# Kernel optimization log

Measured on AMD Instinct MI355X. Metric: run time of the kernel, lower is better.

The kernel has to match this reference:

```python
import jax, jax.numpy as jnp
import numpy as np

N, D, C = 100000, 384, 8


def setup_inputs() -> dict:
    key = jax.random.key(0)
    k1, k2, k3, k4 = jax.random.split(key, 4)
    Y = jax.random.normal(k1, (N, D), dtype=jnp.float32)
    O = jax.random.bernoulli(k2, 0.9, (N, D))  # observation mask
    # learned VB parameters (as held in the nn.Parameters of VBPCA)
    mbar = 0.1 * jax.random.normal(k3, (D,), dtype=jnp.float32)
    wbar = 0.1 * jax.random.normal(k4, (D, C), dtype=jnp.float32)
    Sigmaw = jnp.broadcast_to(jnp.eye(C, dtype=jnp.float32), (D, C, C))
    vy = jnp.float32(1.0)
    return {"Y": Y, "O": O, "mbar": mbar, "wbar": wbar, "Sigmaw": Sigmaw, "vy": vy}


def reference(Y, O, mbar, wbar, Sigmaw, vy):
    O_ = O.astype(Y.dtype)            # [N, D]
    Y = jnp.nan_to_num(Y)
    # per-channel rank-c outer product plus Sigmaw: baddbmm(Sigmaw, wbar[:,:,None], wbar[:,None,:])
    OwwSw = Sigmaw + wbar[:, :, None] * wbar[:, None, :]            # [D, C, C]
    # accumulate over observed channels: [N, D] @ [D, C*C] -> [N, C, C]
    A = (O_ @ OwwSw.reshape(D, C * C)).reshape(-1, C, C)
    Ic = jnp.eye(C, dtype=Y.dtype)
    Sigma_xn = vy * jnp.linalg.inv(vy * Ic[None] + A)               # [N, C, C]
    # xbarn = einsum('nlk,ni,ik,ni->nl', Sigma_xn/vy, O_, wbar, Y - mbar)
    t = O_ * (Y - mbar)                                             # [N, D]
    proj = t @ wbar                                                 # [N, C]
    xbarn = jnp.einsum('nlk,nk->nl', Sigma_xn / vy, proj)           # [N, C]
    return xbarn, Sigma_xn
```

## Files before the change

### kernel.cpp

```cpp
#include <hip/hip_runtime.h>

#define NN 100000
#define DD 384
#define CC 8
#define ROWS 64

typedef unsigned int uint;
typedef _Float16 half8 __attribute__((ext_vector_type(8)));
typedef float floatx4 __attribute__((ext_vector_type(4)));

__device__ __forceinline__ constexpr int TIDX(int i, int j) { return i * (i + 1) / 2 + j; }

__device__ __forceinline__ uint pkh2(float a, float b) {
  return __builtin_bit_cast(uint, __builtin_amdgcn_cvt_pkrtz(a, b));
}

__global__ __launch_bounds__(64) void vbpca_prep(
    const float* __restrict__ wbar, const float* __restrict__ Sigmaw,
    uint4* __restrict__ bfrag) {
  const int l = threadIdx.x;
  const int kt = blockIdx.x;
  const int kgrp = l >> 4;
#pragma unroll
  for (int ct = 0; ct < 3; ++ct) {
    const int col = ct * 16 + (l & 15);
    int ii = 0;
#pragma unroll
    for (int t = 0; t < 7; ++t) {
      if ((ii + 1) * (ii + 2) / 2 <= col && ii < 7) ++ii;
    }
    const int jj = col - ii * (ii + 1) / 2;
    float v[8];
#pragma unroll
    for (int j = 0; j < 8; ++j) {
      const int d = kt * 32 + kgrp * 8 + j;
      float val;
      if (col < 36) {
        val = Sigmaw[(size_t)d * 64 + ii * 8 + jj] + wbar[d * 8 + ii] * wbar[d * 8 + jj];
      } else if (col < 44) {
        val = wbar[d * 8 + (col - 36)];
      } else {
        val = 0.f;
      }
      v[j] = val;
    }
    uint4 u;
    u.x = pkh2(v[0], v[1]); u.y = pkh2(v[2], v[3]);
    u.z = pkh2(v[4], v[5]); u.w = pkh2(v[6], v[7]);
    bfrag[(kt * 3 + ct) * 64 + l] = u;
  }
}

__global__ __launch_bounds__(256, 4) void vbpca_main(
    const float* __restrict__ Y, const int* __restrict__ O,
    const uint4* __restrict__ bfrag, const float* __restrict__ mbar,
    const float* __restrict__ vyp, float* __restrict__ out) {
  __shared__ float smemf[6656];
  float* mbar_l = smemf;
  float* scat_l = smemf + 384;
  float* sigst = smemf + 384;
  float* xbst = smemf + 384 + 4160;

  const int tid = threadIdx.x;
  const int wu = __builtin_amdgcn_readfirstlane((int)(tid >> 6));
  const int l = tid & 63;

  for (int i = tid; i < DD; i += 256) mbar_l[i] = mbar[i];
  __syncthreads();

  const int rt0 = blockIdx.x * ROWS + wu * 16;
  int gr0 = rt0 + ((l & 15) >> 1);
  gr0 = gr0 < NN ? gr0 : NN - 1;
  int gr1 = rt0 + 8 + ((l & 15) >> 1);
  gr1 = gr1 < NN ? gr1 : NN - 1;
  const float tsel = (float)(l & 1);
  const float osel = 1.f - tsel;
  const int kgo = (l >> 4) * 8;

  const float* __restrict__ Yr0 = Y + (size_t)gr0 * DD;
  const int* __restrict__ Or0 = O + (size_t)gr0 * DD;
  const float* __restrict__ Yr1 = Y + (size_t)gr1 * DD;
  const int* __restrict__ Or1 = O + (size_t)gr1 * DD;

  floatx4 accA[3], accB[3];
#pragma unroll
  for (int j = 0; j < 3; ++j) {
    accA[j] = (floatx4){0.f, 0.f, 0.f, 0.f};
    accB[j] = (floatx4){0.f, 0.f, 0.f, 0.f};
  }

#define GATHER_FRAG(YR, OR, KT, FRAG)                                       \
  {                                                                         \
    const int kb = (KT) * 32 + kgo;                                         \
    const float4 ylo = *reinterpret_cast<const float4*>((YR) + kb);         \
    const float4 yhi = *reinterpret_cast<const float4*>((YR) + kb + 4);     \
    const int4 olo = *reinterpret_cast<const int4*>((OR) + kb);             \
    const int4 ohi = *reinterpret_cast<const int4*>((OR) + kb + 4);         \
    const float4 mlo = *reinterpret_cast<const float4*>(mbar_l + kb);       \
    const float4 mhi = *reinterpret_cast<const float4*>(mbar_l + kb + 4);   \
    const float v0 = (float)olo.x * fmaf(tsel, ylo.x - mlo.x, osel);        \
    const float v1 = (float)olo.y * fmaf(tsel, ylo.y - mlo.y, osel);        \
    const float v2 = (float)olo.z * fmaf(tsel, ylo.z - mlo.z, osel);        \
    const float v3 = (float)olo.w * fmaf(tsel, ylo.w - mlo.w, osel);        \
    const float v4 = (float)ohi.x * fmaf(tsel, yhi.x - mhi.x, osel);        \
    const float v5 = (float)ohi.y * fmaf(tsel, yhi.y - mhi.y, osel);        \
    const float v6 = (float)ohi.z * fmaf(tsel, yhi.z - mhi.z, osel);        \
    const float v7 = (float)ohi.w * fmaf(tsel, yhi.w - mhi.w, osel);        \
    uint4 fu;                                                               \
    fu.x = pkh2(v0, v1); fu.y = pkh2(v2, v3);                               \
    fu.z = pkh2(v4, v5); fu.w = pkh2(v6, v7);                               \
    FRAG = __builtin_bit_cast(half8, fu);                                   \
  }

#define MTILE_LOOP(YR, OR, ACC)                                             \
  {                                                                         \
    uint4 bf0 = bfrag[0 * 64 + l];                                          \
    uint4 bf1 = bfrag[1 * 64 + l];                                          \
    uint4 bf2 = bfrag[2 * 64 + l];                                          \
    _Pragma("unroll") for (int kt = 0; kt < 12; ++kt) {                     \
      half8 av;                                                             \
      GATHER_FRAG(YR, OR, kt, av);                                          \
      uint4 nb0, nb1, nb2;                                                  \
      if (kt < 11) {                                                        \
        nb0 = bfrag[((kt + 1) * 3 + 0) * 64 + l];                           \
        nb1 = bfrag[((kt + 1) * 3 + 1) * 64 + l];                           \
        nb2 = bfrag[((kt + 1) * 3 + 2) * 64 + l];                           \
      }                                                                     \
      ACC[0] = __builtin_amdgcn_mfma_f32_16x16x32_f16(                      \
          av, __builtin_bit_cast(half8, bf0), ACC[0], 0, 0, 0);             \
      ACC[1] = __builtin_amdgcn_mfma_f32_16x16x32_f16(                      \
          av, __builtin_bit_cast(half8, bf1), ACC[1], 0, 0, 0);             \
      ACC[2] = __builtin_amdgcn_mfma_f32_16x16x32_f16(                      \
          av, __builtin_bit_cast(half8, bf2), ACC[2], 0, 0, 0);             \
      bf0 = nb0; bf1 = nb1; bf2 = nb2;                                      \
    }                                                                       \
  }

  MTILE_LOOP(Yr0, Or0, accA);
  MTILE_LOOP(Yr1, Or1, accB);

  __syncthreads();

#pragma unroll
  for (int ct = 0; ct < 3; ++ct) {
#pragma unroll
    for (int reg = 0; reg < 4; ++reg) {
      const int m = (l >> 4) * 4 + reg;
      scat_l[(wu * 32 + m) * 49 + ct * 16 + (l & 15)] = accA[ct][reg];
      scat_l[(wu * 32 + 16 + m) * 49 + ct * 16 + (l & 15)] = accB[ct][reg];
    }
  }
  __syncthreads();

  float a[36], pr[CC];
  if (tid < 64) {
#pragma unroll
    for (int k = 0; k < 36; ++k) a[k] = scat_l[(2 * tid) * 49 + k];
#pragma unroll
    for (int j = 0; j < CC; ++j) pr[j] = scat_l[(2 * tid + 1) * 49 + 36 + j];
  }
  __syncthreads();

  if (tid < 64) {
    const int row = tid;
    const float vy = *vyp;

    float L[36];
#pragma unroll
    for (int j = 0; j < CC; ++j) {
      float s = a[TIDX(j, j)] + vy;
#pragma unroll
      for (int k = 0; k < CC; ++k) {
        if (k < j) s -= L[TIDX(j, k)] * L[TIDX(j, k)];
      }
      const float dj = sqrtf(s);
      L[TIDX(j, j)] = dj;
      const float invdj = 1.0f / dj;
#pragma unroll
      for (int i = j + 1; i < CC; ++i) {
        float tt = a[TIDX(i, j)];
#pragma unroll
        for (int k = 0; k < CC; ++k) {
          if (k < j) tt -= L[TIDX(i, k)] * L[TIDX(j, k)];
        }
        L[TIDX(i, j)] = tt * invdj;
      }
    }

    float invd[CC];
#pragma unroll
    for (int i = 0; i < CC; ++i) invd[i] = 1.0f / L[TIDX(i, i)];
    float Li[36];
#pragma unroll
    for (int j = 0; j < CC; ++j) {
      Li[TIDX(j, j)] = invd[j];
#pragma unroll
      for (int i = j + 1; i < CC; ++i) {
        float s = 0.f;
#pragma unroll
        for (int k = 0; k < CC; ++k) {
          if (k >= j && k < i) s += L[TIDX(i, k)] * Li[TIDX(k, j)];
        }
        Li[TIDX(i, j)] = -s * invd[i];
      }
    }

    float sig[36];
#pragma unroll
    for (int i = 0; i < CC; ++i) {
#pragma unroll
      for (int j = 0; j <= i; ++j) {
        float s = 0.f;
#pragma unroll
        for (int k = 0; k < CC; ++k) {
          if (k >= i) s += Li[TIDX(k, i)] * Li[TIDX(k, j)];
        }
        sig[TIDX(i, j)] = vy * s;
      }
    }

    float uvec[CC];
#pragma unroll
    for (int i = 0; i < CC; ++i) {
      float s = 0.f;
#pragma unroll
      for (int j = 0; j < CC; ++j) {
        if (j <= i) s += Li[TIDX(i, j)] * pr[j];
      }
      uvec[i] = s;
    }
#pragma unroll
    for (int ll = 0; ll < CC; ++ll) {
      float s = 0.f;
#pragma unroll
      for (int i = 0; i < CC; ++i) {
        if (i >= ll) s += Li[TIDX(i, ll)] * uvec[i];
      }
      xbst[row * 9 + ll] = s;
    }
#pragma unroll
    for (int i = 0; i < CC; ++i) {
#pragma unroll
      for (int j = 0; j < CC; ++j) {
        sigst[row * 65 + i * 8 + j] = (j <= i) ? sig[TIDX(i, j)] : sig[TIDX(j, i)];
      }
    }
  }
  __syncthreads();

  const int valid = (NN - blockIdx.x * ROWS < ROWS) ? (NN - blockIdx.x * ROWS) : ROWS;
  float* __restrict__ sig_out = out + (size_t)NN * CC + (size_t)blockIdx.x * ROWS * 64;
  for (int f = tid; f < valid * 64; f += 256) {
    sig_out[f] = sigst[(f >> 6) * 65 + (f & 63)];
  }
  float* __restrict__ xb_out = out + (size_t)blockIdx.x * ROWS * CC;
  for (int f = tid; f < valid * 8; f += 256) {
    xb_out[f] = xbst[(f >> 3) * 9 + (f & 7)];
  }
}

extern "C" void kernel_launch(void* const* d_in, const int* in_sizes, int n_in,
                              void* d_out, int out_size, void* d_ws, size_t ws_size,
                              hipStream_t stream) {
  const float* Y = (const float*)d_in[0];
  const int* O = (const int*)d_in[1];
  const float* mbar = (const float*)d_in[2];
  const float* wbar = (const float*)d_in[3];
  const float* Sigmaw = (const float*)d_in[4];
  const float* vyp = (const float*)d_in[5];
  float* out = (float*)d_out;
  uint4* bfrag = (uint4*)d_ws;

  vbpca_prep<<<12, 64, 0, stream>>>(wbar, Sigmaw, bfrag);
  vbpca_main<<<(NN + ROWS - 1) / ROWS, 256, 0, stream>>>(Y, O, bfrag, mbar, vyp, out);
}
```

Baseline: 89.89 us.

## Stage Y and O tiles through LDS with async double-buffered global_load_lds

Each wave used to gather its Y and O fragments straight from global memory inside the MFMA loop. Now the wave's row tiles are prefetched into a per-wave, XOR-swizzled LDS double buffer using async global-to-LDS loads, and fragments are read from LDS. The aim is to overlap global memory latency with MFMA work and to get coalesced 16-byte row loads. In exchange, shared memory grows to about 50KB per block and launch bounds drop to 3 blocks per CU. Correctness depends on the compiler inserting the right vmcnt waits before LDS reads and before each buffer is overwritten.

```diff
diff --git a/kernel.cpp b/kernel.cpp
--- a/kernel.cpp
+++ b/kernel.cpp
@@ -51,15 +51,16 @@
   }
 }
 
-__global__ __launch_bounds__(256, 4) void vbpca_main(
+__global__ __launch_bounds__(256, 3) void vbpca_main(
     const float* __restrict__ Y, const int* __restrict__ O,
     const uint4* __restrict__ bfrag, const float* __restrict__ mbar,
     const float* __restrict__ vyp, float* __restrict__ out) {
-  __shared__ float smemf[6656];
-  float* mbar_l = smemf;
-  float* scat_l = smemf + 384;
-  float* sigst = smemf + 384;
-  float* xbst = smemf + 384 + 4160;
+  __shared__ uint smem[12672];
+  uint* tile = smem;
+  float* mbar_l = (float*)(smem + 12288);
+  float* scat_l = (float*)smem;
+  float* sigst = (float*)smem;
+  float* xbst = (float*)smem + 4160;
 
   const int tid = threadIdx.x;
   const int wu = __builtin_amdgcn_readfirstlane((int)(tid >> 6));
@@ -68,19 +69,31 @@
   for (int i = tid; i < DD; i += 256) mbar_l[i] = mbar[i];
   __syncthreads();
 
+  uint* wbuf = tile + wu * 3072;
   const int rt0 = blockIdx.x * ROWS + wu * 16;
-  int gr0 = rt0 + ((l & 15) >> 1);
-  gr0 = gr0 < NN ? gr0 : NN - 1;
-  int gr1 = rt0 + 8 + ((l & 15) >> 1);
-  gr1 = gr1 < NN ? gr1 : NN - 1;
   const float tsel = (float)(l & 1);
   const float osel = 1.f - tsel;
-  const int kgo = (l >> 4) * 8;
-
-  const float* __restrict__ Yr0 = Y + (size_t)gr0 * DD;
-  const int* __restrict__ Or0 = O + (size_t)gr0 * DD;
-  const float* __restrict__ Yr1 = Y + (size_t)gr1 * DD;
-  const int* __restrict__ Or1 = O + (size_t)gr1 * DD;
+
+#define GLOAD16(GSRC, LDST)                                                  \
+  __builtin_amdgcn_global_load_lds(                                          \
+      (const __attribute__((address_space(1))) void*)(GSRC),                 \
+      (__attribute__((address_space(3))) void*)(LDST), 16, 0, 0)
+
+#define ISSUE(M, S, BUF)                                                     \
+  {                                                                          \
+    _Pragma("unroll") for (int i = 0; i < 3; ++i) {                          \
+      const int p = i * 64 + l;                                              \
+      const int r = p / 24;                                                  \
+      const int c4 = (p - r * 24) ^ (r & 7);                                 \
+      int row = rt0 + (M)*8 + r;                                             \
+      row = row < NN ? row : NN - 1;                                         \
+      const size_t goff = (size_t)row * 96 + (S)*24 + c4;                    \
+      GLOAD16(reinterpret_cast<const float4*>(Y) + goff,                     \
+              wbuf + (BUF)*1536 + i * 256 + l * 4);                          \
+      GLOAD16(reinterpret_cast<const int4*>(O) + goff,                       \
+              wbuf + (BUF)*1536 + 768 + i * 256 + l * 4);                    \
+    }                                                                        \
+  }
 
   floatx4 accA[3], accB[3];
 #pragma unroll
@@ -88,56 +101,82 @@
     accA[j] = (floatx4){0.f, 0.f, 0.f, 0.f};
     accB[j] = (floatx4){0.f, 0.f, 0.f, 0.f};
   }
-
-#define GATHER_FRAG(YR, OR, KT, FRAG)                                       \
-  {                                                                         \
-    const int kb = (KT) * 32 + kgo;                                         \
-    const float4 ylo = *reinterpret_cast<const float4*>((YR) + kb);         \
-    const float4 yhi = *reinterpret_cast<const float4*>((YR) + kb + 4);     \
-    const int4 olo = *reinterpret_cast<const int4*>((OR) + kb);             \
-    const int4 ohi = *reinterpret_cast<const int4*>((OR) + kb + 4);         \
-    const float4 mlo = *reinterpret_cast<const float4*>(mbar_l + kb);       \
-    const float4 mhi = *reinterpret_cast<const float4*>(mbar_l + kb + 4);   \
-    const float v0 = (float)olo.x * fmaf(tsel, ylo.x - mlo.x, osel);        \
-    const float v1 = (float)olo.y * fmaf(tsel, ylo.y - mlo.y, osel);        \
-    const float v2 = (float)olo.z * fmaf(tsel, ylo.z - mlo.z, osel);        \
-    const float v3 = (float)olo.w * fmaf(tsel, ylo.w - mlo.w, osel);        \
-    const float v4 = (float)ohi.x * fmaf(tsel, yhi.x - mhi.x, osel);        \
-    const float v5 = (float)ohi.y * fmaf(tsel, yhi.y - mhi.y, osel);        \
-    const float v6 = (float)ohi.z * fmaf(tsel, yhi.z - mhi.z, osel);        \
-    const float v7 = (float)ohi.w * fmaf(tsel, yhi.w - mhi.w, osel);        \
-    uint4 fu;                                                               \
-    fu.x = pkh2(v0, v1); fu.y = pkh2(v2, v3);                               \
-    fu.z = pkh2(v4, v5); fu.w = pkh2(v6, v7);                               \
-    FRAG = __builtin_bit_cast(half8, fu);                                   \
-  }
-
-#define MTILE_LOOP(YR, OR, ACC)                                             \
-  {                                                                         \
-    uint4 bf0 = bfrag[0 * 64 + l];                                          \
-    uint4 bf1 = bfrag[1 * 64 + l];                                          \
-    uint4 bf2 = bfrag[2 * 64 + l];                                          \
-    _Pragma("unroll") for (int kt = 0; kt < 12; ++kt) {                     \
-      half8 av;                                                             \
-      GATHER_FRAG(YR, OR, kt, av);                                          \
-      uint4 nb0, nb1, nb2;                                                  \
-      if (kt < 11) {                                                        \
-        nb0 = bfrag[((kt + 1) * 3 + 0) * 64 + l];                           \
-        nb1 = bfrag[((kt + 1) * 3 + 1) * 64 + l];                           \
-        nb2 = bfrag[((kt + 1) * 3 + 2) * 64 + l];                           \
-      }                                                                     \
-      ACC[0] = __builtin_amdgcn_mfma_f32_16x16x32_f16(                      \
-          av, __builtin_bit_cast(half8, bf0), ACC[0], 0, 0, 0);             \
-      ACC[1] = __builtin_amdgcn_mfma_f32_16x16x32_f16(                      \
-          av, __builtin_bit_cast(half8, bf1), ACC[1], 0, 0, 0);             \
-      ACC[2] = __builtin_amdgcn_mfma_f32_16x16x32_f16(                      \
-          av, __builtin_bit_cast(half8, bf2), ACC[2], 0, 0, 0);             \
-      bf0 = nb0; bf1 = nb1; bf2 = nb2;                                      \
-    }                                                                       \
-  }
-
-  MTILE_LOOP(Yr0, Or0, accA);
-  MTILE_LOOP(Yr1, Or1, accB);
+  uint4 bf0, bf1, bf2;
+
+#define FRAG(S, J, BUF, AV)                                                  \
+  half8 AV;                                                                  \
+  {                                                                          \
+    const int ktg = (S)*3 + (J);                                             \
+    const int r = (l & 15) >> 1;                                             \
+    const int c4a = (J)*8 + (l >> 4) * 2;                                    \
+    const uint* bb = wbuf + (BUF)*1536;                                      \
+    const float4 ylo = *reinterpret_cast<const float4*>(                     \
+        bb + (r * 24 + ((c4a) ^ (r & 7))) * 4);                              \
+    const float4 yhi = *reinterpret_cast<const float4*>(                     \
+        bb + (r * 24 + ((c4a + 1) ^ (r & 7))) * 4);                          \
+    const int4 olo = *reinterpret_cast<const int4*>(                         \
+        bb + 768 + (r * 24 + ((c4a) ^ (r & 7))) * 4);                        \
+    const int4 ohi = *reinterpret_cast<const int4*>(                         \
+        bb + 768 + (r * 24 + ((c4a + 1) ^ (r & 7))) * 4);                    \
+    const float4 mlo =                                                       \
+        *reinterpret_cast<const float4*>(mbar_l + ktg * 32 + (l >> 4) * 8);  \
+    const float4 mhi = *reinterpret_cast<const float4*>(                     \
+        mbar_l + ktg * 32 + (l >> 4) * 8 + 4);                               \
+    const float v0 = (float)olo.x * fmaf(tsel, ylo.x - mlo.x, osel);         \
+    const float v1 = (float)olo.y * fmaf(tsel, ylo.y - mlo.y, osel);         \
+    const float v2 = (float)olo.z * fmaf(tsel, ylo.z - mlo.z, osel);         \
+    const float v3 = (float)olo.w * fmaf(tsel, ylo.w - mlo.w, osel);         \
+    const float v4 = (float)ohi.x * fmaf(tsel, yhi.x - mhi.x, osel);         \
+    const float v5 = (float)ohi.y * fmaf(tsel, yhi.y - mhi.y, osel);         \
+    const float v6 = (float)ohi.z * fmaf(tsel, yhi.z - mhi.z, osel);         \
+    const float v7 = (float)ohi.w * fmaf(tsel, yhi.w - mhi.w, osel);         \
+    uint4 fu;                                                                \
+    fu.x = pkh2(v0, v1); fu.y = pkh2(v2, v3);                                \
+    fu.z = pkh2(v4, v5); fu.w = pkh2(v6, v7);                                \
+    AV = __builtin_bit_cast(half8, fu);                                      \
+  }
+
+#define KT_BODY(S, J, BUF, ACC)                                              \
+  {                                                                          \
+    FRAG(S, J, BUF, av);                                                     \
+    const int ktn = (S)*3 + (J) + 1;                                         \
+    uint4 nb0, nb1, nb2;                                                     \
+    if (ktn < 12) {                                                          \
+      nb0 = bfrag[(ktn * 3 + 0) * 64 + l];                                   \
+      nb1 = bfrag[(ktn * 3 + 1) * 64 + l];                                   \
+      nb2 = bfrag[(ktn * 3 + 2) * 64 + l];                                   \
+    }                                                                        \
+    ACC[0] = __builtin_amdgcn_mfma_f32_16x16x32_f16(                         \
+        av, __builtin_bit_cast(half8, bf0), ACC[0], 0, 0, 0);                \
+    ACC[1] = __builtin_amdgcn_mfma_f32_16x16x32_f16(                         \
+        av, __builtin_bit_cast(half8, bf1), ACC[1], 0, 0, 0);                \
+    ACC[2] = __builtin_amdgcn_mfma_f32_16x16x32_f16(                         \
+        av, __builtin_bit_cast(half8, bf2), ACC[2], 0, 0, 0);                \
+    bf0 = nb0; bf1 = nb1; bf2 = nb2;                                         \
+  }
+
+#define BPRELOAD()                                                           \
+  bf0 = bfrag[0 * 64 + l];                                                   \
+  bf1 = bfrag[1 * 64 + l];                                                   \
+  bf2 = bfrag[2 * 64 + l];
+
+#define STEP(S, BUF, ACC)                                                    \
+  KT_BODY(S, 0, BUF, ACC);                                                   \
+  KT_BODY(S, 1, BUF, ACC);                                                   \
+  KT_BODY(S, 2, BUF, ACC);
+
+  ISSUE(0, 0, 0);
+  ISSUE(0, 1, 1);
+  BPRELOAD();
+  STEP(0, 0, accA);  ISSUE(0, 2, 0);
+  STEP(1, 1, accA);  ISSUE(0, 3, 1);
+  STEP(2, 0, accA);  ISSUE(1, 0, 0);
+  STEP(3, 1, accA);  ISSUE(1, 1, 1);
+  BPRELOAD();
+  STEP(0, 0, accB);  ISSUE(1, 2, 0);
+  STEP(1, 1, accB);  ISSUE(1, 3, 1);
+  STEP(2, 0, accB);
+  STEP(3, 1, accB);
 
   __syncthreads();
 
```

Result: slower. 94.13 us (+4.7%).

## Split MFMA accumulation and per-row Cholesky solve into separate kernels

Applied to the files above, without the earlier changes.

The fused kernel is split in two. The MFMA reduction kernel now handles 32 rows per block, writes the 44 packed moments per row to a workspace buffer, and declares higher occupancy through launch bounds. A second kernel reads the workspace and runs the 8x8 Cholesky inverse and the projection, 64 rows per block. This removes the serial single-wave solve tail from the bandwidth-bound MFMA kernel and allows more concurrent blocks. The cost is an extra kernel launch plus a round trip of about 19 MB through global memory.

```diff
diff --git a/kernel.cpp b/kernel.cpp
--- a/kernel.cpp
+++ b/kernel.cpp
@@ -3,7 +3,6 @@
 #define NN 100000
 #define DD 384
 #define CC 8
-#define ROWS 64
 
 typedef unsigned int uint;
 typedef _Float16 half8 __attribute__((ext_vector_type(8)));
@@ -51,16 +50,11 @@
   }
 }
 
-__global__ __launch_bounds__(256, 4) void vbpca_main(
+__global__ __launch_bounds__(256, 8) void vbpca_mfma(
     const float* __restrict__ Y, const int* __restrict__ O,
     const uint4* __restrict__ bfrag, const float* __restrict__ mbar,
-    const float* __restrict__ vyp, float* __restrict__ out) {
-  __shared__ float smemf[6656];
-  float* mbar_l = smemf;
-  float* scat_l = smemf + 384;
-  float* sigst = smemf + 384;
-  float* xbst = smemf + 384 + 4160;
-
+    float* __restrict__ cws) {
+  __shared__ float mbar_l[DD];
   const int tid = threadIdx.x;
   const int wu = __builtin_amdgcn_readfirstlane((int)(tid >> 6));
   const int l = tid & 63;
@@ -68,102 +62,100 @@
   for (int i = tid; i < DD; i += 256) mbar_l[i] = mbar[i];
   __syncthreads();
 
-  const int rt0 = blockIdx.x * ROWS + wu * 16;
-  int gr0 = rt0 + ((l & 15) >> 1);
-  gr0 = gr0 < NN ? gr0 : NN - 1;
-  int gr1 = rt0 + 8 + ((l & 15) >> 1);
-  gr1 = gr1 < NN ? gr1 : NN - 1;
+  const int R0 = blockIdx.x * 32 + wu * 8;
+  const int gr = R0 + ((l & 15) >> 1);
   const float tsel = (float)(l & 1);
   const float osel = 1.f - tsel;
   const int kgo = (l >> 4) * 8;
 
-  const float* __restrict__ Yr0 = Y + (size_t)gr0 * DD;
-  const int* __restrict__ Or0 = O + (size_t)gr0 * DD;
-  const float* __restrict__ Yr1 = Y + (size_t)gr1 * DD;
-  const int* __restrict__ Or1 = O + (size_t)gr1 * DD;
-
-  floatx4 accA[3], accB[3];
-#pragma unroll
-  for (int j = 0; j < 3; ++j) {
-    accA[j] = (floatx4){0.f, 0.f, 0.f, 0.f};
-    accB[j] = (floatx4){0.f, 0.f, 0.f, 0.f};
-  }
-
-#define GATHER_FRAG(YR, OR, KT, FRAG)                                       \
-  {                                                                         \
-    const int kb = (KT) * 32 + kgo;                                         \
-    const float4 ylo = *reinterpret_cast<const float4*>((YR) + kb);         \
-    const float4 yhi = *reinterpret_cast<const float4*>((YR) + kb + 4);     \
-    const int4 olo = *reinterpret_cast<const int4*>((OR) + kb);             \
-    const int4 ohi = *reinterpret_cast<const int4*>((OR) + kb + 4);         \
-    const float4 mlo = *reinterpret_cast<const float4*>(mbar_l + kb);       \
-    const float4 mhi = *reinterpret_cast<const float4*>(mbar_l + kb + 4);   \
-    const float v0 = (float)olo.x * fmaf(tsel, ylo.x - mlo.x, osel);        \
-    const float v1 = (float)olo.y * fmaf(tsel, ylo.y - mlo.y, osel);        \
-    const float v2 = (float)olo.z * fmaf(tsel, ylo.z - mlo.z, osel);        \
-    const float v3 = (float)olo.w * fmaf(tsel, ylo.w - mlo.w, osel);        \
-    const float v4 = (float)ohi.x * fmaf(tsel, yhi.x - mhi.x, osel);        \
-    const float v5 = (float)ohi.y * fmaf(tsel, yhi.y - mhi.y, osel);        \
-    const float v6 = (float)ohi.z * fmaf(tsel, yhi.z - mhi.z, osel);        \
-    const float v7 = (float)ohi.w * fmaf(tsel, yhi.w - mhi.w, osel);        \
-    uint4 fu;                                                               \
-    fu.x = pkh2(v0, v1); fu.y = pkh2(v2, v3);                               \
-    fu.z = pkh2(v4, v5); fu.w = pkh2(v6, v7);                               \
-    FRAG = __builtin_bit_cast(half8, fu);                                   \
-  }
-
-#define MTILE_LOOP(YR, OR, ACC)                                             \
-  {                                                                         \
-    uint4 bf0 = bfrag[0 * 64 + l];                                          \
-    uint4 bf1 = bfrag[1 * 64 + l];                                          \
-    uint4 bf2 = bfrag[2 * 64 + l];                                          \
-    _Pragma("unroll") for (int kt = 0; kt < 12; ++kt) {                     \
-      half8 av;                                                             \
-      GATHER_FRAG(YR, OR, kt, av);                                          \
-      uint4 nb0, nb1, nb2;                                                  \
-      if (kt < 11) {                                                        \
-        nb0 = bfrag[((kt + 1) * 3 + 0) * 64 + l];                           \
-        nb1 = bfrag[((kt + 1) * 3 + 1) * 64 + l];                           \
-        nb2 = bfrag[((kt + 1) * 3 + 2) * 64 + l];                           \
-      }                                                                     \
-      ACC[0] = __builtin_amdgcn_mfma_f32_16x16x32_f16(                      \
-          av, __builtin_bit_cast(half8, bf0), ACC[0], 0, 0, 0);             \
-      ACC[1] = __builtin_amdgcn_mfma_f32_16x16x32_f16(                      \
-          av, __builtin_bit_cast(half8, bf1), ACC[1], 0, 0, 0);             \
-      ACC[2] = __builtin_amdgcn_mfma_f32_16x16x32_f16(                      \
-          av, __builtin_bit_cast(half8, bf2), ACC[2], 0, 0, 0);             \
-      bf0 = nb0; bf1 = nb1; bf2 = nb2;                                      \
-    }                                                                       \
-  }
-
-  MTILE_LOOP(Yr0, Or0, accA);
-  MTILE_LOOP(Yr1, Or1, accB);
-
-  __syncthreads();
-
-#pragma unroll
-  for (int ct = 0; ct < 3; ++ct) {
-#pragma unroll
-    for (int reg = 0; reg < 4; ++reg) {
-      const int m = (l >> 4) * 4 + reg;
-      scat_l[(wu * 32 + m) * 49 + ct * 16 + (l & 15)] = accA[ct][reg];
-      scat_l[(wu * 32 + 16 + m) * 49 + ct * 16 + (l & 15)] = accB[ct][reg];
-    }
-  }
-  __syncthreads();
-
-  float a[36], pr[CC];
-  if (tid < 64) {
-#pragma unroll
-    for (int k = 0; k < 36; ++k) a[k] = scat_l[(2 * tid) * 49 + k];
-#pragma unroll
-    for (int j = 0; j < CC; ++j) pr[j] = scat_l[(2 * tid + 1) * 49 + 36 + j];
+  const float* __restrict__ Yr = Y + (size_t)gr * DD;
+  const int* __restrict__ Or = O + (size_t)gr * DD;
+
+  floatx4 acc[3];
+#pragma unroll
+  for (int j = 0; j < 3; ++j) acc[j] = (floatx4){0.f, 0.f, 0.f, 0.f};
+
+  uint4 bf0 = bfrag[0 * 64 + l];
+  uint4 bf1 = bfrag[1 * 64 + l];
+  uint4 bf2 = bfrag[2 * 64 + l];
+#pragma unroll
+  for (int kt = 0; kt < 12; ++kt) {
+    const int kb = kt * 32 + kgo;
+    const float4 ylo = *reinterpret_cast<const float4*>(Yr + kb);
+    const float4 yhi = *reinterpret_cast<const float4*>(Yr + kb + 4);
+    const int4 olo = *reinterpret_cast<const int4*>(Or + kb);
+    const int4 ohi = *reinterpret_cast<const int4*>(Or + kb + 4);
+    const float4 mlo = *reinterpret_cast<const float4*>(mbar_l + kb);
+    const float4 mhi = *reinterpret_cast<const float4*>(mbar_l + kb + 4);
+    const float v0 = (float)olo.x * fmaf(tsel, ylo.x - mlo.x, osel);
+    const float v1 = (float)olo.y * fmaf(tsel, ylo.y - mlo.y, osel);
+    const float v2 = (float)olo.z * fmaf(tsel, ylo.z - mlo.z, osel);
+    const float v3 = (float)olo.w * fmaf(tsel, ylo.w - mlo.w, osel);
+    const float v4 = (float)ohi.x * fmaf(tsel, yhi.x - mhi.x, osel);
+    const float v5 = (float)ohi.y * fmaf(tsel, yhi.y - mhi.y, osel);
+    const float v6 = (float)ohi.z * fmaf(tsel, yhi.z - mhi.z, osel);
+    const float v7 = (float)ohi.w * fmaf(tsel, yhi.w - mhi.w, osel);
+    uint4 fu;
+    fu.x = pkh2(v0, v1); fu.y = pkh2(v2, v3);
+    fu.z = pkh2(v4, v5); fu.w = pkh2(v6, v7);
+    const half8 av = __builtin_bit_cast(half8, fu);
+    uint4 nb0, nb1, nb2;
+    if (kt < 11) {
+      nb0 = bfrag[((kt + 1) * 3 + 0) * 64 + l];
+      nb1 = bfrag[((kt + 1) * 3 + 1) * 64 + l];
+      nb2 = bfrag[((kt + 1) * 3 + 2) * 64 + l];
+    }
+    acc[0] = __builtin_amdgcn_mfma_f32_16x16x32_f16(
+        av, __builtin_bit_cast(half8, bf0), acc[0], 0, 0, 0);
+    acc[1] = __builtin_amdgcn_mfma_f32_16x16x32_f16(
+        av, __builtin_bit_cast(half8, bf1), acc[1], 0, 0, 0);
+    acc[2] = __builtin_amdgcn_mfma_f32_16x16x32_f16(
+        av, __builtin_bit_cast(half8, bf2), acc[2], 0, 0, 0);
+    bf0 = nb0; bf1 = nb1; bf2 = nb2;
+  }
+
+  const int lm = l & 15;
+  const int g2 = (l >> 4) * 2;
+#pragma unroll
+  for (int reg = 0; reg < 4; ++reg) {
+    float* wr = cws + (size_t)(R0 + g2 + (reg >> 1)) * 48;
+    if ((reg & 1) == 0) {
+      wr[0 * 16 + lm] = acc[0][reg];
+      wr[1 * 16 + lm] = acc[1][reg];
+      if (lm < 4) wr[2 * 16 + lm] = acc[2][reg];
+    } else {
+      if (lm >= 4 && lm < 12) wr[2 * 16 + lm] = acc[2][reg];
+    }
+  }
+}
+
+__global__ __launch_bounds__(256) void vbpca_solve(
+    const float* __restrict__ cws, const float* __restrict__ vyp,
+    float* __restrict__ out) {
+  __shared__ float stg[64 * 48];
+  __shared__ float sigst[64 * 65];
+  __shared__ float xbst[64 * 9];
+
+  const int tid = threadIdx.x;
+  const int base = blockIdx.x * 64;
+
+  float4* stg4 = reinterpret_cast<float4*>(stg);
+  const float4* cws4 = reinterpret_cast<const float4*>(cws);
+  for (int f = tid; f < 768; f += 256) {
+    int rr = base + f / 12;
+    rr = rr < NN ? rr : NN - 1;
+    stg4[f] = cws4[(size_t)rr * 12 + (f % 12)];
   }
   __syncthreads();
 
   if (tid < 64) {
     const int row = tid;
     const float vy = *vyp;
+    float a[36], pr[CC];
+#pragma unroll
+    for (int k = 0; k < 36; ++k) a[k] = stg[row * 48 + k];
+#pragma unroll
+    for (int j = 0; j < CC; ++j) pr[j] = stg[row * 48 + 36 + j];
 
     float L[36];
 #pragma unroll
@@ -248,12 +240,12 @@
   }
   __syncthreads();
 
-  const int valid = (NN - blockIdx.x * ROWS < ROWS) ? (NN - blockIdx.x * ROWS) : ROWS;
-  float* __restrict__ sig_out = out + (size_t)NN * CC + (size_t)blockIdx.x * ROWS * 64;
+  const int valid = (NN - base < 64) ? (NN - base) : 64;
+  float* __restrict__ sig_out = out + (size_t)NN * CC + (size_t)base * 64;
   for (int f = tid; f < valid * 64; f += 256) {
     sig_out[f] = sigst[(f >> 6) * 65 + (f & 63)];
   }
-  float* __restrict__ xb_out = out + (size_t)blockIdx.x * ROWS * CC;
+  float* __restrict__ xb_out = out + (size_t)base * CC;
   for (int f = tid; f < valid * 8; f += 256) {
     xb_out[f] = xbst[(f >> 3) * 9 + (f & 7)];
   }
@@ -270,7 +262,9 @@
   const float* vyp = (const float*)d_in[5];
   float* out = (float*)d_out;
   uint4* bfrag = (uint4*)d_ws;
+  float* cws = (float*)((char*)d_ws + 36864);
 
   vbpca_prep<<<12, 64, 0, stream>>>(wbar, Sigmaw, bfrag);
-  vbpca_main<<<(NN + ROWS - 1) / ROWS, 256, 0, stream>>>(Y, O, bfrag, mbar, vyp, out);
-}
+  vbpca_mfma<<<NN / 32, 256, 0, stream>>>(Y, O, bfrag, mbar, cws);
+  vbpca_solve<<<(NN + 63) / 64, 256, 0, stream>>>(cws, vyp, out);
+}
```

Measured after the change: 112.6 us. 25.2% more time.
